# Performance work log

Measured on AMD Instinct MI355X. Metric: run time of the kernel, lower is better.

## Reference

```python
import jax, jax.numpy as jnp
import numpy as np

D_MODEL, D_STATE, EXPAND = 1024, 128, 2
E = D_MODEL * EXPAND          # 2048
N = D_STATE                   # 128
H = 1
P = E
TD = D_STATE // 2             # 64
Z_DIM = E + E + N + N + H + H + TD + H  # 4369
EPS = 1e-05
B_SZ, L = 4, 2048


def setup_inputs() -> dict:
    key = jax.random.key(0)
    ks = jax.random.split(key, 6)
    u = jax.random.normal(ks[0], (B_SZ, L, D_MODEL), dtype=jnp.float32)
    W_in = jax.random.normal(ks[1], (Z_DIM, D_MODEL), dtype=jnp.float32) * 0.02
    W_out = jax.random.normal(ks[2], (D_MODEL, E), dtype=jnp.float32) * 0.02
    w_normB = jnp.ones((N,), jnp.float32)
    w_normC = jnp.ones((N,), jnp.float32)
    B_bias = jnp.ones((N,), jnp.float32)
    C_bias = jnp.ones((N,), jnp.float32)
    # dt_bias buffer: dt_i ~ logU(0.001, 0.1); dt_bias = dt_i + log(-expm1(-dt_i))
    dt_i = jnp.exp(jax.random.uniform(ks[3], (H,)) * (np.log(0.1) - np.log(0.001)) + np.log(0.001))
    dt_i = jnp.clip(dt_i, 1e-4, None)
    dt_bias = dt_i + jnp.log(-jnp.expm1(-dt_i))
    A_log = jnp.full((H,), np.log(0.5), jnp.float32)
    return {"u": u, "W_in": W_in, "w_normB": w_normB, "w_normC": w_normC,
            "B_bias": B_bias, "C_bias": C_bias, "dt_bias": dt_bias,
            "A_log": A_log, "W_out": W_out}


def _rms(x, w):
    return x * jax.lax.rsqrt(jnp.mean(x * x, axis=-1, keepdims=True) + EPS) * w


def _rope(x, ang):
    half = x.shape[-1] // 2
    x1, x2 = x[..., :half], x[..., half:]
    c, s = jnp.cos(ang), jnp.sin(ang)
    return jnp.concatenate([x1 * c - x2 * s, x1 * s + x2 * c], axis=-1)


def reference(u, W_in, w_normB, w_normC, B_bias, C_bias, dt_bias, A_log, W_out):
    Bb, Ls, _ = u.shape
    z = u @ W_in.T  # [B, L, Z_DIM]
    o = 0
    def take(n):
        nonlocal o
        r = z[..., o:o + n]; o += n; return r
    x = jax.nn.silu(take(E))
    gate = jax.nn.silu(take(E))
    B_ = take(N)
    C_ = take(N)
    dt_ = take(H)
    A_ = take(H)
    th = take(TD)
    lam_ = take(H)

    dt = jax.nn.softplus(dt_ + dt_bias)          # [B, L, H]
    A = -jax.nn.softplus(A_ + A_log)             # [B, L, H]
    lam = jax.nn.sigmoid(lam_)                   # [B, L, H]
    alpha = jnp.exp(dt * A)                      # [B, L, H]

    B_ = _rms(B_, w_normB) + B_bias
    C_ = _rms(C_, w_normC) + C_bias
    ca = jnp.cumsum(jnp.mean(dt, axis=-1, keepdims=True) * th, axis=1)  # [B, L, TD]
    B_ = _rope(B_, ca)
    C_ = _rope(C_, ca)

    xh = x.reshape(Bb, Ls, H, P)
    xp = jnp.concatenate([jnp.zeros_like(xh[:, :1]), xh[:, :-1]], axis=1)  # roll + zero t=0
    lh = lam[..., None]
    xt = lh * xh + (1.0 - lh) * alpha[..., None] * xp  # [B, L, H, P]

    # fallback SSM: per-channel mean drive, per-head scalar A (mean over batch+time)
    u_mean = jnp.mean(xt, axis=-1)               # [B, L, H]
    A_bar = jnp.mean(A, axis=(0, 1))             # [H]
    dA = jnp.exp(dt * A_bar)                     # [B, L, H]
    dBu = dt[..., None] * B_[:, :, None, :] * u_mean[..., None]  # [B, L, H, N]

    def step(state, xs):
        dA_t, dBu_t, C_t = xs                    # [B,H], [B,H,N], [B,N]
        state = dA_t[..., None] * state + dBu_t  # [B, H, N]
        y_t = jnp.einsum('bhn,bn->bh', state, C_t)
        return state, y_t

    state0 = jnp.zeros((Bb, H, N), dtype=xt.dtype)
    _, ys = jax.lax.scan(step, state0,
                         (jnp.moveaxis(dA, 1, 0), jnp.moveaxis(dBu, 1, 0), jnp.moveaxis(C_, 1, 0)))
    outs = jnp.moveaxis(ys, 0, 1)                # [B, L, H]
    y = jnp.broadcast_to(outs, (Bb, Ls, E))      # H=1 expanded to E
    return (y * gate) @ W_out.T
```

## Files before the change

### kernel.cpp

```cpp
#include <hip/hip_runtime.h>
#include <cstdint>
#include <cstddef>

typedef __bf16 bf16_t;
typedef bf16_t bf16x8 __attribute__((ext_vector_type(8)));
typedef bf16_t bf16x4 __attribute__((ext_vector_type(4)));
typedef float f32x4 __attribute__((ext_vector_type(4)));

#define B_SZ    4
#define LSEQ    2048
#define DMODEL  1024
#define EDIM    2048
#define ZDIM    4419
#define ZPAD    4608
#define ROWS    (B_SZ*LSEQ)
#define EPSV    1e-5f

#define LDU     1088
#define LDG     2112

#define SCHUNK  128
#define SCLEN   (LSEQ/SCHUNK)
#define RCH     128
#define RCLEN   (LSEQ/RCH)

__device__ __forceinline__ float softplus_f(float x){
  return fmaxf(x, 0.f) + log1pf(expf(-fabsf(x)));
}
__device__ __forceinline__ float sigmoid_f(float x){ return 1.f/(1.f+expf(-x)); }
__device__ __forceinline__ float silu_f(float x){ return x/(1.f+expf(-x)); }

__device__ __forceinline__ void gload_lds16(const void* g, void* l){
  __builtin_amdgcn_global_load_lds(
      (const __attribute__((address_space(1))) void*)g,
      (__attribute__((address_space(3))) void*)l, 16, 0, 0);
}

__device__ __forceinline__ float blockReduce128(float v, float* red, int t){
  red[t] = v; __syncthreads();
  #pragma unroll
  for (int off = 64; off > 0; off >>= 1){
    if (t < off) red[t] += red[t+off];
    __syncthreads();
  }
  float r = red[0];
  __syncthreads();
  return r;
}

__global__ __launch_bounds__(256) void prep_kernel(
    const float4* __restrict__ u4, const float4* __restrict__ win4,
    const float4* __restrict__ wout4,
    bf16_t* __restrict__ ubf, bf16_t* __restrict__ winbf, bf16_t* __restrict__ woutbf,
    float* __restrict__ Asum, float* __restrict__ xraw)
{
  size_t i = (size_t)blockIdx.x*256 + threadIdx.x;
  if (i == 0) Asum[0] = 0.f;
  if (i < ROWS) xraw[i] = 0.f;
  const size_t NU4 = (size_t)ROWS*DMODEL/4;
  const size_t NW4 = (size_t)ZPAD*DMODEL/4;
  const size_t NO4 = (size_t)DMODEL*EDIM/4;
  if (i < NU4){
    float4 v = u4[i];
    size_t e = i*4, row = e>>10, col = e&1023;
    bf16x4 o = { (bf16_t)v.x, (bf16_t)v.y, (bf16_t)v.z, (bf16_t)v.w };
    *(bf16x4*)&ubf[row*LDU + col] = o;
    return;
  }
  i -= NU4;
  if (i < NW4){
    size_t e = i*4, row = e>>10, col = e&1023;
    bf16x4 o;
    if (row < (size_t)ZDIM){
      float4 v = win4[i];
      o = bf16x4{ (bf16_t)v.x, (bf16_t)v.y, (bf16_t)v.z, (bf16_t)v.w };
    } else {
      o = bf16x4{ (bf16_t)0.f, (bf16_t)0.f, (bf16_t)0.f, (bf16_t)0.f };
    }
    *(bf16x4*)&winbf[row*LDU + col] = o;
    return;
  }
  i -= NW4;
  if (i < NO4){
    float4 v = wout4[i];
    size_t e = i*4, row = e>>11, col = e&2047;
    bf16x4 o = { (bf16_t)v.x, (bf16_t)v.y, (bf16_t)v.z, (bf16_t)v.w };
    *(bf16x4*)&woutbf[row*LDG + col] = o;
  }
}

template<int LDA_, int LDW_, int NT, int NXT, int MODE>
__global__ __launch_bounds__(256, 3) void gemmS_kernel(
    const bf16_t* __restrict__ A0, const bf16_t* __restrict__ W0,
    float* __restrict__ xraw, bf16_t* __restrict__ o_g, float* __restrict__ o_z,
    const float* __restrict__ scale, float* __restrict__ o_f)
{
  __shared__ __align__(16) bf16_t lds[(256+128)*32];

  const int tid = threadIdx.x;
  const int wid = tid>>6, lane = tid&63;
  const int wr = wid>>1, wc = wid&1;
  const int lr = lane&15, hi = lane>>4;

  constexpr int NWG = NXT*(ROWS/256);
  const int id = blockIdx.x;
  const int rid = (id & 7)*(NWG/8) + (id>>3);
  const int bx = rid % NXT, by = rid / NXT;
  const int m0 = by*256, n0 = bx*128;

  f32x4 acc[8][4] = {};

  int gAoff[4], lAoff[4], gBoff[2], lBoff[2];
  #pragma unroll
  for (int q = 0; q < 4; ++q){
    int cidx = q*256 + tid;
    int row = cidx>>2, ch = cidx&3;
    int sc = ch ^ (row&3) ^ ((row>>2)&3);
    gAoff[q] = row*LDA_ + sc*8;
    lAoff[q] = cidx*8;
  }
  #pragma unroll
  for (int q = 0; q < 2; ++q){
    int cidx = q*256 + tid;
    int row = cidx>>2, ch = cidx&3;
    int sc = ch ^ (row&3) ^ ((row>>2)&3);
    gBoff[q] = row*LDW_ + sc*8;
    lBoff[q] = 8192 + cidx*8;
  }
  int aoff[8], boff[4];
  #pragma unroll
  for (int m = 0; m < 8; ++m){
    int row = wr*128 + m*16 + lr;
    int sc = hi ^ (row&3) ^ ((row>>2)&3);
    aoff[m] = row*32 + sc*8;
  }
  #pragma unroll
  for (int n = 0; n < 4; ++n){
    int row = wc*64 + n*16 + lr;
    int sc = hi ^ (row&3) ^ ((row>>2)&3);
    boff[n] = 8192 + row*32 + sc*8;
  }

  const bf16_t* Ak = A0 + (size_t)m0*LDA_;
  const bf16_t* Wk = W0 + (size_t)n0*LDW_;

  #pragma unroll 1
  for (int t = 0; t < NT; ++t){
    #pragma unroll
    for (int q = 0; q < 4; ++q) gload_lds16(Ak + gAoff[q], &lds[lAoff[q]]);
    #pragma unroll
    for (int q = 0; q < 2; ++q) gload_lds16(Wk + gBoff[q], &lds[lBoff[q]]);
    Ak += 32; Wk += 32;
    __syncthreads();
    bf16x8 bfr[4];
    #pragma unroll
    for (int n = 0; n < 4; ++n) bfr[n] = *(const bf16x8*)&lds[boff[n]];
    #pragma unroll
    for (int m = 0; m < 8; ++m){
      bf16x8 af = *(const bf16x8*)&lds[aoff[m]];
      #pragma unroll
      for (int n = 0; n < 4; ++n)
        acc[m][n] = __builtin_amdgcn_mfma_f32_16x16x32_bf16(af, bfr[n], acc[m][n], 0,0,0);
    }
    __syncthreads();
  }

  if (MODE == 0 && n0 < 2048){
    #pragma unroll
    for (int m = 0; m < 8; ++m){
      #pragma unroll
      for (int i = 0; i < 4; ++i){
        float p = 0.f;
        #pragma unroll
        for (int n = 0; n < 4; ++n) p += silu_f(acc[m][n][i]);
        p += __shfl_xor(p, 8); p += __shfl_xor(p, 4);
        p += __shfl_xor(p, 2); p += __shfl_xor(p, 1);
        if (lr == 0){
          int r = m0 + wr*128 + m*16 + (hi<<2) + i;
          atomicAdd(xraw + r, p);
        }
      }
    }
  } else if (MODE == 0){
    #pragma unroll
    for (int m = 0; m < 8; ++m){
      int rowb = m0 + wr*128 + m*16 + (hi<<2);
      #pragma unroll
      for (int n = 0; n < 4; ++n){
        int col = n0 + wc*64 + n*16 + lr;
        #pragma unroll
        for (int i = 0; i < 4; ++i){
          int r = rowb + i;
          float v = acc[m][n][i];
          if (col < 4096)      o_g[(size_t)r*LDG + (col-2048)] = (bf16_t)silu_f(v);
          else if (col < 4480) o_z[(size_t)r*384 + (col-4096)] = v;
        }
      }
    }
  } else {
    #pragma unroll
    for (int m = 0; m < 8; ++m){
      int rowb = m0 + wr*128 + m*16 + (hi<<2);
      #pragma unroll
      for (int i = 0; i < 4; ++i){
        int r = rowb + i;
        float s = scale[r];
        #pragma unroll
        for (int n = 0; n < 4; ++n){
          int col = n0 + wc*64 + n*16 + lr;
          o_f[(size_t)r*DMODEL + col] = acc[m][n][i]*s;
        }
      }
    }
  }
}

__global__ __launch_bounds__(128) void fuse_kernel(
    const float* __restrict__ xraw, const float* __restrict__ zs,
    const float* __restrict__ wnB, const float* __restrict__ wnC,
    const float* __restrict__ Bb, const float* __restrict__ Cb,
    const float* __restrict__ dtb, const float* __restrict__ Alog,
    float* __restrict__ Bn, float* __restrict__ Cn, float* __restrict__ dtth,
    float* __restrict__ dts, float* __restrict__ alphas, float* __restrict__ lams,
    float* __restrict__ xbar, float* Asum)
{
  __shared__ float red[128];
  int r = blockIdx.x, t = threadIdx.x;
  const float* zr = zs + (size_t)r*384;
  float bv = zr[t], cv = zr[128+t];
  float b2 = blockReduce128(bv*bv, red, t);
  float c2 = blockReduce128(cv*cv, red, t);
  float rb = rsqrtf(b2*(1.f/128.f) + EPSV);
  float rc = rsqrtf(c2*(1.f/128.f) + EPSV);
  Bn[(size_t)r*128 + t] = bv*rb*wnB[t] + Bb[t];
  Cn[(size_t)r*128 + t] = cv*rc*wnC[t] + Cb[t];

  float dt = softplus_f(zr[256] + dtb[0]);
  if (t < 64) dtth[(size_t)r*64 + t] = dt * zr[258+t];
  if (t == 0){
    float Av  = -softplus_f(zr[257] + Alog[0]);
    float lam = sigmoid_f(zr[322]);
    dts[r]    = dt;
    alphas[r] = expf(dt*Av);
    lams[r]   = lam;
    xbar[r]   = xraw[r] * (1.f/2048.f);
    atomicAdd(Asum, Av);
  }
}

__global__ __launch_bounds__(64) void rope_sum_kernel(
    const float* __restrict__ dtth, float* __restrict__ csum)
{
  int b  = blockIdx.x >> 7;
  int ch = blockIdx.x & 127;
  int d  = threadIdx.x;
  const float* base = dtth + ((size_t)b*LSEQ + (size_t)ch*RCLEN)*64 + d;
  float s = 0.f;
  #pragma unroll
  for (int i = 0; i < RCLEN; ++i) s += base[(size_t)i*64];
  csum[((size_t)b*RCH + ch)*64 + d] = s;
}

__global__ __launch_bounds__(64) void rope_prefix_kernel(float* __restrict__ csum)
{
  int b = blockIdx.x, d = threadIdx.x;
  float s = 0.f;
  for (int c = 0; c < RCH; ++c){
    size_t idx = ((size_t)b*RCH + c)*64 + d;
    float v = csum[idx]; csum[idx] = s; s += v;
  }
}

__global__ __launch_bounds__(64) void rope_apply_kernel(
    const float* __restrict__ dtth, const float* __restrict__ csum,
    float* __restrict__ Bn, float* __restrict__ Cn)
{
  int b  = blockIdx.x >> 7;
  int ch = blockIdx.x & 127;
  int d  = threadIdx.x;
  float ca = csum[((size_t)b*RCH + ch)*64 + d];
  int l0 = ch*RCLEN;
  const float* base = dtth + ((size_t)b*LSEQ)*64 + d;
  for (int l = l0; l < l0 + RCLEN; ++l){
    ca += base[(size_t)l*64];
    float sn, cs;
    sincosf(ca, &sn, &cs);
    size_t ro = ((size_t)b*LSEQ + l)*128;
    float b1 = Bn[ro+d], b2v = Bn[ro+64+d];
    Bn[ro+d]    = b1*cs - b2v*sn;
    Bn[ro+64+d] = b1*sn + b2v*cs;
    float c1 = Cn[ro+d], c2v = Cn[ro+64+d];
    Cn[ro+d]    = c1*cs - c2v*sn;
    Cn[ro+64+d] = c1*sn + c2v*cs;
  }
}

__global__ __launch_bounds__(64) void scan_local_kernel(
    const float* __restrict__ dts, const float* __restrict__ alphas,
    const float* __restrict__ lams, const float* __restrict__ xbar,
    const float* __restrict__ Asum,
    const float* __restrict__ Bn, const float* __restrict__ Cn,
    float* __restrict__ ylocal, float* __restrict__ Pfix,
    float* __restrict__ Sfin, float* __restrict__ Dch)
{
  int b  = blockIdx.x / SCHUNK;
  int ch = blockIdx.x % SCHUNK;
  int n  = threadIdx.x;
  float Abar = Asum[0] * (1.f/(float)ROWS);
  float s1 = 0.f, s2 = 0.f, P = 1.f;
  int l0 = ch*SCLEN;
  #pragma unroll
  for (int i = 0; i < SCLEN; ++i){
    int l = l0 + i;
    size_t r = (size_t)b*LSEQ + l;
    float dt = dts[r], lam = lams[r], al = alphas[r], xb = xbar[r];
    float xp = (l > 0) ? xbar[r-1] : 0.f;
    float um = lam*xb + (1.f-lam)*al*xp;
    float dA = expf(dt*Abar);
    float coef = dt*um;
    size_t ro = r*128;
    s1 = dA*s1 + coef*Bn[ro+n];
    s2 = dA*s2 + coef*Bn[ro+64+n];
    P *= dA;
    float p = s1*Cn[ro+n] + s2*Cn[ro+64+n];
    #pragma unroll
    for (int off = 32; off > 0; off >>= 1) p += __shfl_down(p, off);
    if (n == 0){ ylocal[r] = p; Pfix[r] = P; }
  }
  size_t so = ((size_t)b*SCHUNK + ch)*128;
  Sfin[so + n]      = s1;
  Sfin[so + 64 + n] = s2;
  if (n == 0) Dch[b*SCHUNK + ch] = P;
}

__global__ __launch_bounds__(128) void scan_carry_kernel(
    const float* __restrict__ Sfin, const float* __restrict__ Dch,
    float* __restrict__ Sin)
{
  int b = blockIdx.x;
  int n = threadIdx.x;
  float s = 0.f;
  for (int c = 0; c < SCHUNK; ++c){
    size_t so = ((size_t)b*SCHUNK + c)*128;
    Sin[so + n] = s;
    s = Dch[b*SCHUNK + c]*s + Sfin[so + n];
  }
}

__global__ __launch_bounds__(256) void scan_fix_kernel(
    const float* __restrict__ Cn, const float* __restrict__ Sin,
    const float* __restrict__ ylocal, const float* __restrict__ Pfix,
    float* __restrict__ outsv)
{
  int r = blockIdx.x*4 + (threadIdx.x>>6);
  int n = threadIdx.x & 63;
  int b  = r / LSEQ;
  int ch = (r % LSEQ) / SCLEN;
  const float* si = Sin + ((size_t)b*SCHUNK + ch)*128;
  size_t ro = (size_t)r*128;
  float p = Cn[ro+n]*si[n] + Cn[ro+64+n]*si[64+n];
  #pragma unroll
  for (int off = 32; off > 0; off >>= 1) p += __shfl_down(p, off);
  if (n == 0) outsv[r] = ylocal[r] + Pfix[r]*p;
}

extern "C" void kernel_launch(void* const* d_in, const int* in_sizes, int n_in,
                              void* d_out, int out_size, void* d_ws, size_t ws_size,
                              hipStream_t stream)
{
  const float* u    = (const float*)d_in[0];
  const float* W_in = (const float*)d_in[1];
  const float* wnB  = (const float*)d_in[2];
  const float* wnC  = (const float*)d_in[3];
  const float* Bb   = (const float*)d_in[4];
  const float* Cb   = (const float*)d_in[5];
  const float* dtb  = (const float*)d_in[6];
  const float* Alog = (const float*)d_in[7];
  const float* Wout = (const float*)d_in[8];
  float* out = (float*)d_out;
  char* ws = (char*)d_ws;

  constexpr size_t OFF_ASUM = 0;
  constexpr size_t OFF_UBF  = 256;
  constexpr size_t SZ_UBF   = (size_t)ROWS*LDU*2;
  constexpr size_t OFF_WIN  = OFF_UBF + SZ_UBF;
  constexpr size_t SZ_WIN   = (size_t)ZPAD*LDU*2;
  constexpr size_t OFF_WOUT = OFF_WIN + SZ_WIN;
  constexpr size_t SZ_WOUT  = (size_t)DMODEL*LDG*2;
  constexpr size_t OFF_G    = OFF_WOUT + SZ_WOUT;
  constexpr size_t SZ_G     = (size_t)ROWS*LDG*2;
  constexpr size_t OFF_ZS   = OFF_G + SZ_G;
  constexpr size_t SZ_ZS    = (size_t)ROWS*384*4;
  constexpr size_t OFF_BN   = OFF_ZS + SZ_ZS;
  constexpr size_t SZ_BN    = (size_t)ROWS*128*4;
  constexpr size_t OFF_CN   = OFF_BN + SZ_BN;
  constexpr size_t OFF_DTTH = OFF_CN + SZ_BN;
  constexpr size_t SZ_DTTH  = (size_t)ROWS*64*4;
  constexpr size_t OFF_XRAW = OFF_DTTH + SZ_DTTH;
  constexpr size_t OFF_DT   = OFF_XRAW + (size_t)ROWS*4;
  constexpr size_t OFF_AL   = OFF_DT  + (size_t)ROWS*4;
  constexpr size_t OFF_LAM  = OFF_AL  + (size_t)ROWS*4;
  constexpr size_t OFF_XB   = OFF_LAM + (size_t)ROWS*4;
  constexpr size_t OFF_OUTS = OFF_XB  + (size_t)ROWS*4;
  constexpr size_t OFF_YLOC = OFF_OUTS + (size_t)ROWS*4;
  constexpr size_t OFF_PFIX = OFF_YLOC + (size_t)ROWS*4;
  constexpr size_t OFF_SFIN = OFF_PFIX + (size_t)ROWS*4;
  constexpr size_t SZ_SFIN  = (size_t)B_SZ*SCHUNK*128*4;
  constexpr size_t OFF_DCH  = OFF_SFIN + SZ_SFIN;
  constexpr size_t OFF_SIN  = OFF_DCH + (size_t)B_SZ*SCHUNK*4;
  constexpr size_t OFF_CSUM = OFF_SIN + SZ_SFIN;

  float*  Asum   = (float*) (ws + OFF_ASUM);
  bf16_t* ubf    = (bf16_t*)(ws + OFF_UBF);
  bf16_t* winbf  = (bf16_t*)(ws + OFF_WIN);
  bf16_t* woutbf = (bf16_t*)(ws + OFF_WOUT);
  bf16_t* gbuf   = (bf16_t*)(ws + OFF_G);
  float*  zsb    = (float*) (ws + OFF_ZS);
  float*  Bn     = (float*) (ws + OFF_BN);
  float*  Cn     = (float*) (ws + OFF_CN);
  float*  dtth   = (float*) (ws + OFF_DTTH);
  float*  xraw   = (float*) (ws + OFF_XRAW);
  float*  dts    = (float*) (ws + OFF_DT);
  float*  alphas = (float*) (ws + OFF_AL);
  float*  lams   = (float*) (ws + OFF_LAM);
  float*  xbar   = (float*) (ws + OFF_XB);
  float*  outsv  = (float*) (ws + OFF_OUTS);
  float*  ylocal = (float*) (ws + OFF_YLOC);
  float*  Pfix   = (float*) (ws + OFF_PFIX);
  float*  Sfin   = (float*) (ws + OFF_SFIN);
  float*  Dch    = (float*) (ws + OFF_DCH);
  float*  Sin    = (float*) (ws + OFF_SIN);
  float*  csum   = (float*) (ws + OFF_CSUM);

  {
    size_t total4 = ((size_t)ROWS*DMODEL + (size_t)ZPAD*DMODEL + (size_t)DMODEL*EDIM)/4;
    int blocks = (int)((total4 + 255)/256);
    prep_kernel<<<blocks, 256, 0, stream>>>(
        (const float4*)u, (const float4*)W_in, (const float4*)Wout,
        ubf, winbf, woutbf, Asum, xraw);
  }
  gemmS_kernel<LDU, LDU, 32, ZPAD/128, 0>
      <<<(ZPAD/128)*(ROWS/256), 256, 0, stream>>>(
      ubf, winbf, xraw, gbuf, zsb, nullptr, nullptr);
  fuse_kernel<<<ROWS, 128, 0, stream>>>(xraw, zsb, wnB, wnC, Bb, Cb, dtb, Alog,
                                        Bn, Cn, dtth, dts, alphas, lams, xbar, Asum);
  rope_sum_kernel<<<B_SZ*RCH, 64, 0, stream>>>(dtth, csum);
  rope_prefix_kernel<<<B_SZ, 64, 0, stream>>>(csum);
  rope_apply_kernel<<<B_SZ*RCH, 64, 0, stream>>>(dtth, csum, Bn, Cn);
  scan_local_kernel<<<B_SZ*SCHUNK, 64, 0, stream>>>(dts, alphas, lams, xbar, Asum,
                                                    Bn, Cn, ylocal, Pfix, Sfin, Dch);
  scan_carry_kernel<<<B_SZ, 128, 0, stream>>>(Sfin, Dch, Sin);
  scan_fix_kernel<<<ROWS/4, 256, 0, stream>>>(Cn, Sin, ylocal, Pfix, outsv);
  gemmS_kernel<LDG, LDG, 64, DMODEL/128, 1>
      <<<(DMODEL/128)*(ROWS/256), 256, 0, stream>>>(
      gbuf, woutbf, nullptr, nullptr, nullptr, outsv, out);
}
```

Baseline: 353.3 us.

## Read A fragments straight from global and split output GEMM along K

The GEMM kernel is restructured. A operands are now loaded straight from global memory into registers, and only W is staged through a larger swizzled LDS buffer in chunks of 256 along K. This removes the LDS round-trip for A and cuts barriers to one pair per chunk. The output GEMM is split two ways along K, and partial results are combined with atomicAdd into a zero-filled output, which doubles the workgroup count. The cost is uncoalesced direct global A loads, lower occupancy (launch bounds 2), a memset, and atomic traffic on the output.

```diff
diff --git a/kernel.cpp b/kernel.cpp
--- a/kernel.cpp
+++ b/kernel.cpp
@@ -89,80 +89,77 @@
   }
 }
 
-template<int LDA_, int LDW_, int NT, int NXT, int MODE>
-__global__ __launch_bounds__(256, 3) void gemmS_kernel(
+template<int LDA_, int LDW_, int NCH, int NXT, int MODE>
+__global__ __launch_bounds__(256, 2) void gemmAD_kernel(
     const bf16_t* __restrict__ A0, const bf16_t* __restrict__ W0,
     float* __restrict__ xraw, bf16_t* __restrict__ o_g, float* __restrict__ o_z,
     const float* __restrict__ scale, float* __restrict__ o_f)
 {
-  __shared__ __align__(16) bf16_t lds[(256+128)*32];
+  __shared__ __align__(16) bf16_t ldsB[32768];
 
   const int tid = threadIdx.x;
   const int wid = tid>>6, lane = tid&63;
   const int wr = wid>>1, wc = wid&1;
   const int lr = lane&15, hi = lane>>4;
-
-  constexpr int NWG = NXT*(ROWS/256);
+  const int hv = hi*16;
+  const int swz = (lr&7)<<4;
+
+  constexpr int NWG = (MODE==0) ? NXT*(ROWS/256) : NXT*(ROWS/256)*2;
   const int id = blockIdx.x;
   const int rid = (id & 7)*(NWG/8) + (id>>3);
-  const int bx = rid % NXT, by = rid / NXT;
+  int bx, by, kz = 0;
+  if (MODE == 0){ bx = rid % NXT; by = rid / NXT; }
+  else { kz = rid / (NXT*(ROWS/256)); int r2 = rid % (NXT*(ROWS/256));
+         bx = r2 % NXT; by = r2 / NXT; }
   const int m0 = by*256, n0 = bx*128;
 
   f32x4 acc[8][4] = {};
 
-  int gAoff[4], lAoff[4], gBoff[2], lBoff[2];
-  #pragma unroll
-  for (int q = 0; q < 4; ++q){
-    int cidx = q*256 + tid;
-    int row = cidx>>2, ch = cidx&3;
-    int sc = ch ^ (row&3) ^ ((row>>2)&3);
-    gAoff[q] = row*LDA_ + sc*8;
-    lAoff[q] = cidx*8;
-  }
-  #pragma unroll
-  for (int q = 0; q < 2; ++q){
-    int cidx = q*256 + tid;
-    int row = cidx>>2, ch = cidx&3;
-    int sc = ch ^ (row&3) ^ ((row>>2)&3);
-    gBoff[q] = row*LDW_ + sc*8;
-    lBoff[q] = 8192 + cidx*8;
-  }
-  int aoff[8], boff[4];
-  #pragma unroll
-  for (int m = 0; m < 8; ++m){
-    int row = wr*128 + m*16 + lr;
-    int sc = hi ^ (row&3) ^ ((row>>2)&3);
-    aoff[m] = row*32 + sc*8;
-  }
-  #pragma unroll
-  for (int n = 0; n < 4; ++n){
-    int row = wc*64 + n*16 + lr;
-    int sc = hi ^ (row&3) ^ ((row>>2)&3);
-    boff[n] = 8192 + row*32 + sc*8;
-  }
-
-  const bf16_t* Ak = A0 + (size_t)m0*LDA_;
-  const bf16_t* Wk = W0 + (size_t)n0*LDW_;
+  const bf16_t* pa[8];
+  #pragma unroll
+  for (int m = 0; m < 8; ++m)
+    pa[m] = A0 + (size_t)(m0 + wr*128 + m*16 + lr)*LDA_ + (size_t)kz*1024 + hv/2;
+
+  int gwoff[16];
+  #pragma unroll
+  for (int q = 0; q < 16; ++q){
+    int c = q*256 + tid;
+    int row = c>>5, wi = (c&31)*16;
+    gwoff[q] = (n0+row)*LDW_ + ((wi ^ ((row&7)<<4))>>1);
+  }
+  const bf16_t* Wb = W0 + (size_t)kz*1024;
+  int rowbase[4];
+  #pragma unroll
+  for (int n = 0; n < 4; ++n)
+    rowbase[n] = (wc*64 + n*16 + lr)*512;
 
   #pragma unroll 1
-  for (int t = 0; t < NT; ++t){
-    #pragma unroll
-    for (int q = 0; q < 4; ++q) gload_lds16(Ak + gAoff[q], &lds[lAoff[q]]);
-    #pragma unroll
-    for (int q = 0; q < 2; ++q) gload_lds16(Wk + gBoff[q], &lds[lBoff[q]]);
-    Ak += 32; Wk += 32;
+  for (int c = 0; c < NCH; ++c){
     __syncthreads();
-    bf16x8 bfr[4];
-    #pragma unroll
-    for (int n = 0; n < 4; ++n) bfr[n] = *(const bf16x8*)&lds[boff[n]];
-    #pragma unroll
-    for (int m = 0; m < 8; ++m){
-      bf16x8 af = *(const bf16x8*)&lds[aoff[m]];
+    #pragma unroll
+    for (int q = 0; q < 16; ++q)
+      gload_lds16(Wb + gwoff[q], &ldsB[(q*256 + tid)*8]);
+    Wb += 256;
+    asm volatile("s_waitcnt vmcnt(0)" ::: "memory");
+    __syncthreads();
+
+    #pragma unroll
+    for (int ks = 0; ks < 8; ++ks){
+      bf16x8 bfr[4];
+      const int ksv = ks*64 + hv;
       #pragma unroll
       for (int n = 0; n < 4; ++n)
-        acc[m][n] = __builtin_amdgcn_mfma_f32_16x16x32_bf16(af, bfr[n], acc[m][n], 0,0,0);
+        bfr[n] = *(const bf16x8*)((const char*)ldsB + rowbase[n] + (ksv ^ swz));
+      #pragma unroll
+      for (int m = 0; m < 8; ++m){
+        bf16x8 af = *(const bf16x8*)(pa[m] + ks*32);
+        #pragma unroll
+        for (int n = 0; n < 4; ++n)
+          acc[m][n] = __builtin_amdgcn_mfma_f32_16x16x32_bf16(af, bfr[n], acc[m][n], 0,0,0);
+      }
     }
-    __syncthreads();
+    #pragma unroll
+    for (int m = 0; m < 8; ++m) pa[m] += 256;
   }
 
   if (MODE == 0 && n0 < 2048){
@@ -208,7 +205,7 @@
         #pragma unroll
         for (int n = 0; n < 4; ++n){
           int col = n0 + wc*64 + n*16 + lr;
-          o_f[(size_t)r*DMODEL + col] = acc[m][n][i]*s;
+          atomicAdd(o_f + (size_t)r*DMODEL + col, acc[m][n][i]*s);
         }
       }
     }
@@ -439,7 +436,9 @@
         (const float4*)u, (const float4*)W_in, (const float4*)Wout,
         ubf, winbf, woutbf, Asum, xraw);
   }
-  gemmS_kernel<LDU, LDU, 32, ZPAD/128, 0>
+  hipMemsetAsync(out, 0, (size_t)ROWS*DMODEL*sizeof(float), stream);
+
+  gemmAD_kernel<LDU, LDU, 4, ZPAD/128, 0>
       <<<(ZPAD/128)*(ROWS/256), 256, 0, stream>>>(
       ubf, winbf, xraw, gbuf, zsb, nullptr, nullptr);
   fuse_kernel<<<ROWS, 128, 0, stream>>>(xraw, zsb, wnB, wnC, Bb, Cb, dtb, Alog,
@@ -451,7 +450,7 @@
                                                     Bn, Cn, ylocal, Pfix, Sfin, Dch);
   scan_carry_kernel<<<B_SZ, 128, 0, stream>>>(Sfin, Dch, Sin);
   scan_fix_kernel<<<ROWS/4, 256, 0, stream>>>(Cn, Sin, ylocal, Pfix, outsv);
-  gemmS_kernel<LDG, LDG, 64, DMODEL/128, 1>
-      <<<(DMODEL/128)*(ROWS/256), 256, 0, stream>>>(
+  gemmAD_kernel<LDG, LDG, 4, DMODEL/128, 1>
+      <<<2*(DMODEL/128)*(ROWS/256), 256, 0, stream>>>(
       gbuf, woutbf, nullptr, nullptr, nullptr, outsv, out);
 }
```

After: 553.2 us. 1.57x slower.
